# Kernel optimization log

Hardware: AMD Instinct MI355X
Metric: run time of the kernel (lower is better)

Reference implementation:

```python
import jax, jax.numpy as jnp
import numpy as np

N = 100000
E = 1600000
NIN = 128
NOUT = 128


def setup_inputs() -> dict:
    key = jax.random.key(0)
    k1, k2, k3, k4 = jax.random.split(key, 4)
    x = jax.random.normal(k1, (N, NIN), dtype=jnp.float32)
    edge_index = jax.random.randint(k2, (2, E), 0, N, dtype=jnp.int64)
    edge_attr = jnp.ones((E,), dtype=jnp.float32)  # unused by GCNConv
    # PyG Linear weight is [out, in]; glorot-ish init
    W = jax.random.normal(k3, (NOUT, NIN), dtype=jnp.float32) / np.sqrt(NIN)
    b = jnp.zeros((NOUT,), dtype=jnp.float32)
    return {"x": x, "edge_index": edge_index, "edge_attr": edge_attr, "W": W, "b": b}


def reference(x, edge_index, edge_attr, W, b):
    # PyG GCNConv: add self-loops, symmetric degree normalization,
    # linear transform, scatter-add aggregation at destination, + bias.
    n = x.shape[0]
    loops = jnp.arange(n, dtype=edge_index.dtype)
    src = jnp.concatenate([edge_index[0], loops])  # [E+N]
    dst = jnp.concatenate([edge_index[1], loops])  # [E+N]
    # degree over destination (col) including self-loops, edge weight = 1
    deg = jax.ops.segment_sum(jnp.ones_like(dst, dtype=x.dtype), dst, num_segments=n)
    dinv = jnp.where(deg > 0, jax.lax.rsqrt(deg), 0.0)
    norm = dinv[src] * dinv[dst]  # [E+N]
    h = x @ W.T  # [N, NOUT]
    msg = h[src] * norm[:, None]  # [E+N, NOUT]
    out = jax.ops.segment_sum(msg, dst, num_segments=n)  # [N, NOUT]
    return out + b
```

## Files before the change

kernel.cpp:

```cpp
#include <hip/hip_runtime.h>

#define TPB 256
#define NBLK 256
#define BSH 8

typedef __attribute__((ext_vector_type(4))) float f32x4;
typedef __attribute__((ext_vector_type(8))) short short8;

__device__ __forceinline__ unsigned short f2bf(float f) {
    unsigned u = __float_as_uint(f);
    u = (u + 0x7fffu + ((u >> 16) & 1u)) >> 16;
    return (unsigned short)u;
}
__device__ __forceinline__ float bflo(unsigned u) { return __uint_as_float(u << 16); }
__device__ __forceinline__ float bfhi(unsigned u) { return __uint_as_float(u & 0xffff0000u); }


__global__ __launch_bounds__(256) void k_bhist(const int* __restrict__ dst,
                                               int* __restrict__ btotal, int E, int NB) {
    __shared__ int sh[512];
    for (int i = threadIdx.x; i < NB; i += 256) sh[i] = 0;
    __syncthreads();
    int chunk = (E + NBLK - 1) / NBLK;
    int lo = blockIdx.x * chunk;
    int hi = min(E, lo + chunk);
    for (int e = lo + threadIdx.x; e < hi; e += 256)
        atomicAdd(&sh[dst[e] >> BSH], 1);
    __syncthreads();
    for (int i = threadIdx.x; i < NB; i += 256)
        if (sh[i]) atomicAdd(&btotal[i], sh[i]);
}


__global__ __launch_bounds__(512) void k_bscan(const int* __restrict__ btotal,
                                               int* __restrict__ bbase, int* __restrict__ bcur,
                                               int* __restrict__ offsets, int E, int NB, int N) {
    __shared__ int tmp[2][512];
    int t = threadIdx.x;
    int v = (t < NB) ? btotal[t] : 0;
    tmp[0][t] = v;
    __syncthreads();
    int sb = 0;
    for (int d = 1; d < 512; d <<= 1) {
        int val = tmp[sb][t];
        if (t >= d) val += tmp[sb][t - d];
        tmp[sb ^ 1][t] = val;
        sb ^= 1;
        __syncthreads();
    }
    int excl = tmp[sb][t] - v;
    if (t < NB) { bbase[t] = excl; bcur[t] = excl; }
    if (t == 0) { bbase[NB] = E; offsets[N] = E; }
}


__global__ __launch_bounds__(256) void k_bscatter(const int* __restrict__ src,
                                                  const int* __restrict__ dst,
                                                  int* __restrict__ bcur,
                                                  int2* __restrict__ pairs, int E, int NB) {
    __shared__ int sh[512];
    __shared__ int sbase[512];
    for (int i = threadIdx.x; i < NB; i += 256) sh[i] = 0;
    __syncthreads();
    int chunk = (E + NBLK - 1) / NBLK;
    int lo = blockIdx.x * chunk;
    int hi = min(E, lo + chunk);
    for (int e = lo + threadIdx.x; e < hi; e += 256)
        atomicAdd(&sh[dst[e] >> BSH], 1);
    __syncthreads();
    for (int i = threadIdx.x; i < NB; i += 256) {
        int c = sh[i];
        sbase[i] = c ? atomicAdd(&bcur[i], c) : 0;
    }
    __syncthreads();
    for (int i = threadIdx.x; i < NB; i += 256) sh[i] = sbase[i];
    __syncthreads();
    for (int e = lo + threadIdx.x; e < hi; e += 256) {
        int d = dst[e];
        int pos = atomicAdd(&sh[d >> BSH], 1);
        pairs[pos] = make_int2(d, src[e]);
    }
}


__global__ __launch_bounds__(256) void k_bcsr(const int2* __restrict__ pairs,
                                              const int* __restrict__ bbase,
                                              int* __restrict__ offsets,
                                              int* __restrict__ sorted_src,
                                              float* __restrict__ dinv, int N) {
    __shared__ int hist[256];
    __shared__ int tmp[2][256];
    __shared__ int scur[256];
    int b = blockIdx.x;
    int s0 = bbase[b], s1 = bbase[b + 1];
    int t = threadIdx.x;
    hist[t] = 0;
    __syncthreads();
    for (int e = s0 + t; e < s1; e += 256)
        atomicAdd(&hist[pairs[e].x & 255], 1);
    __syncthreads();
    int v = hist[t];
    tmp[0][t] = v;
    __syncthreads();
    int sb = 0;
    for (int d = 1; d < 256; d <<= 1) {
        int val = tmp[sb][t];
        if (t >= d) val += tmp[sb][t - d];
        tmp[sb ^ 1][t] = val;
        sb ^= 1;
        __syncthreads();
    }
    int gbase = s0 + (tmp[sb][t] - v);
    scur[t] = gbase;
    int d = (b << BSH) + t;
    if (d < N) { offsets[d] = gbase; dinv[d] = rsqrtf((float)v + 1.0f); }
    __syncthreads();
    for (int e = s0 + t; e < s1; e += 256) {
        int2 pr = pairs[e];
        int pos = atomicAdd(&scur[pr.x & 255], 1);
        sorted_src[pos] = pr.y;
    }
}


__global__ void k_castW(const float* __restrict__ W, unsigned short* __restrict__ Wt) {
    int i = blockIdx.x * TPB + threadIdx.x;
    if (i < 128 * 128) Wt[i] = f2bf(W[i]);
}


__global__ __launch_bounds__(256) void k_gemm(const float* __restrict__ x,
                                              const unsigned short* __restrict__ Wt,
                                              const float* __restrict__ dinv,
                                              unsigned short* __restrict__ g, int n) {
    __shared__ unsigned short wb[128][136];
    const int tid = threadIdx.x;

    for (int chunk = tid; chunk < 2048; chunk += 256) {
        int nrow = chunk >> 4, k8 = (chunk & 15) << 3;
        *(uint4*)&wb[nrow][k8] = ((const uint4*)Wt)[chunk];
    }
    __syncthreads();

    const int lane = tid & 63;
    const int wid  = tid >> 6;
    const int l15  = lane & 15;
    const int quad = lane >> 4;
    const int row  = blockIdx.x * 64 + wid * 16 + l15;
    const int rowc = (row < n) ? row : (n - 1);

    f32x4 acc[8];
    #pragma unroll
    for (int t = 0; t < 8; ++t) acc[t] = (f32x4){0.f, 0.f, 0.f, 0.f};

    #pragma unroll
    for (int ks = 0; ks < 4; ++ks) {
        const int kb = ks * 32 + quad * 8;
        float4 a0 = *(const float4*)(x + (long)rowc * 128 + kb);
        float4 a1 = *(const float4*)(x + (long)rowc * 128 + kb + 4);
        union { unsigned short u[8]; short8 v; } af;
        af.u[0] = f2bf(a0.x); af.u[1] = f2bf(a0.y); af.u[2] = f2bf(a0.z); af.u[3] = f2bf(a0.w);
        af.u[4] = f2bf(a1.x); af.u[5] = f2bf(a1.y); af.u[6] = f2bf(a1.z); af.u[7] = f2bf(a1.w);
        #pragma unroll
        for (int t = 0; t < 8; ++t) {
            short8 bf = *(const short8*)&wb[t * 16 + l15][kb];
            acc[t] = __builtin_amdgcn_mfma_f32_16x16x32_bf16(af.v, bf, acc[t], 0, 0, 0);
        }
    }

    int   orow[4];
    float dv[4];
    #pragma unroll
    for (int r = 0; r < 4; ++r) {
        orow[r] = blockIdx.x * 64 + wid * 16 + quad * 4 + r;
        dv[r]   = (orow[r] < n) ? dinv[orow[r]] : 0.f;
    }
    #pragma unroll
    for (int t = 0; t < 8; ++t) {
        int col = t * 16 + l15;
        #pragma unroll
        for (int r = 0; r < 4; ++r) {
            if (orow[r] < n)
                g[(long)orow[r] * 128 + col] = f2bf(acc[t][r] * dv[r]);
        }
    }
}


__global__ __launch_bounds__(256) void k_aggregate(const int* __restrict__ sorted_src,
                                                   const int* __restrict__ offsets,
                                                   const unsigned short* __restrict__ g,
                                                   const float* __restrict__ dinv,
                                                   const float* __restrict__ b,
                                                   float* __restrict__ out, int n) {
    int d = blockIdx.x * (TPB / 32) + (threadIdx.x >> 5);
    if (d >= n) return;
    int c = (threadIdx.x & 31) << 2;

    int s0 = offsets[d];
    int s1 = offsets[d + 1];

    float4 acc = make_float4(0.f, 0.f, 0.f, 0.f);
    auto addrow = [&](int r) {
        uint2 p = *(const uint2*)(g + (long)r * 128 + c);
        acc.x += bflo(p.x); acc.y += bfhi(p.x);
        acc.z += bflo(p.y); acc.w += bfhi(p.y);
    };

    addrow(d);
    int e = s0;
    for (; e + 8 <= s1; e += 8) {
        int a[8];
        #pragma unroll
        for (int j = 0; j < 8; ++j) a[j] = sorted_src[e + j];
        #pragma unroll
        for (int j = 0; j < 8; ++j) addrow(a[j]);
    }
    for (; e + 4 <= s1; e += 4) {
        int a[4];
        #pragma unroll
        for (int j = 0; j < 4; ++j) a[j] = sorted_src[e + j];
        #pragma unroll
        for (int j = 0; j < 4; ++j) addrow(a[j]);
    }
    for (; e < s1; ++e) addrow(sorted_src[e]);

    float s = dinv[d];
    float4 bb = *(const float4*)(b + c);
    float4 r = make_float4(acc.x * s + bb.x, acc.y * s + bb.y,
                           acc.z * s + bb.z, acc.w * s + bb.w);
    *(float4*)(out + (long)d * 128 + c) = r;
}


extern "C" void kernel_launch(void* const* d_in, const int* in_sizes, int n_in,
                              void* d_out, int out_size, void* d_ws, size_t ws_size,
                              hipStream_t stream) {
    const float* x  = (const float*)d_in[0];
    const int*   ei = (const int*)d_in[1];
    const float* W  = (const float*)d_in[3];
    const float* b  = (const float*)d_in[4];
    float* out = (float*)d_out;

    const int N = in_sizes[0] / 128;
    const int E = in_sizes[1] / 2;
    const int* src = ei;
    const int* dst = ei + E;
    const int NB = (N + 255) >> BSH;

    char* p = (char*)d_ws;
    auto carve = [&](size_t bytes) { char* q = p; p += (bytes + 255) & ~(size_t)255; return q; };
    int*            btotal     = (int*)           carve(512 * 4);
    int*            bbase      = (int*)           carve(513 * 4);
    int*            bcur       = (int*)           carve(512 * 4);
    int*            offsets    = (int*)           carve((size_t)(N + 1) * 4);
    float*          dinv       = (float*)         carve((size_t)N * 4);
    int2*           pairs      = (int2*)          carve((size_t)E * 8);
    int*            sorted_src = (int*)           carve((size_t)E * 4);
    unsigned short* Wt         = (unsigned short*)carve((size_t)128 * 128 * 2);
    unsigned short* g          = (unsigned short*)carve((size_t)N * 128 * 2);

    hipMemsetAsync(btotal, 0, 512 * 4, stream);

    k_bhist   <<<NBLK, TPB, 0, stream>>>(dst, btotal, E, NB);
    k_bscan   <<<1, 512, 0, stream>>>(btotal, bbase, bcur, offsets, E, NB, N);
    k_bscatter<<<NBLK, TPB, 0, stream>>>(src, dst, bcur, pairs, E, NB);
    k_bcsr    <<<NB, TPB, 0, stream>>>(pairs, bbase, offsets, sorted_src, dinv, N);

    k_castW<<<(128 * 128 + TPB - 1) / TPB, TPB, 0, stream>>>(W, Wt);
    k_gemm<<<(N + 63) / 64, TPB, 0, stream>>>(x, Wt, dinv, g, N);

    k_aggregate<<<(N + (TPB / 32) - 1) / (TPB / 32), TPB, 0, stream>>>(
        sorted_src, offsets, g, dinv, b, out, N);
}
```

Measured before the change: 254.6 us.

## Drop memset and castW launches; per-block histograms; unroll aggregate by 16

The bucket histogram now writes per-block rows to a workspace that the scan kernel reduces, which removes the global atomics and the memset launch. The separate weight-cast kernel is removed and each GEMM block converts W to bf16 while loading it into shared memory. The aggregation inner loop now prefetches 16 neighbour indices per iteration instead of 8. Together these cut two launches and some atomics, in exchange for redundant W conversion in every GEMM block and a serial 256-row reduction in the single-block scan.

After: 254.9 us. About the same (+0.1%).

```diff
diff --git a/kernel.cpp b/kernel.cpp
--- a/kernel.cpp
+++ b/kernel.cpp
@@ -17,40 +17,44 @@
 
 
 __global__ __launch_bounds__(256) void k_bhist(const int* __restrict__ dst,
-                                               int* __restrict__ btotal, int E, int NB) {
+                                               int* __restrict__ blockhist, int E) {
     __shared__ int sh[512];
-    for (int i = threadIdx.x; i < NB; i += 256) sh[i] = 0;
+    int t = threadIdx.x;
+    sh[t] = 0; sh[t + 256] = 0;
     __syncthreads();
     int chunk = (E + NBLK - 1) / NBLK;
     int lo = blockIdx.x * chunk;
     int hi = min(E, lo + chunk);
-    for (int e = lo + threadIdx.x; e < hi; e += 256)
+    for (int e = lo + t; e < hi; e += 256)
         atomicAdd(&sh[dst[e] >> BSH], 1);
     __syncthreads();
-    for (int i = threadIdx.x; i < NB; i += 256)
-        if (sh[i]) atomicAdd(&btotal[i], sh[i]);
-}
-
-
-__global__ __launch_bounds__(512) void k_bscan(const int* __restrict__ btotal,
+    int* row = blockhist + blockIdx.x * 512;
+    row[t] = sh[t];
+    row[t + 256] = sh[t + 256];
+}
+
+
+__global__ __launch_bounds__(512) void k_bscan(const int* __restrict__ blockhist,
                                                int* __restrict__ bbase, int* __restrict__ bcur,
-                                               int* __restrict__ offsets, int E, int NB, int N) {
+                                               int* __restrict__ offsets, int E, int N) {
     __shared__ int tmp[2][512];
     int t = threadIdx.x;
-    int v = (t < NB) ? btotal[t] : 0;
-    tmp[0][t] = v;
+    int total = 0;
+    #pragma unroll 8
+    for (int b = 0; b < NBLK; ++b) total += blockhist[b * 512 + t];
+    tmp[0][t] = total;
     __syncthreads();
     int sb = 0;
     for (int d = 1; d < 512; d <<= 1) {
-        int val = tmp[sb][t];
-        if (t >= d) val += tmp[sb][t - d];
+        int val = tmp[sb][t] + ((t >= d) ? tmp[sb][t - d] : 0);
         tmp[sb ^ 1][t] = val;
         sb ^= 1;
         __syncthreads();
     }
-    int excl = tmp[sb][t] - v;
-    if (t < NB) { bbase[t] = excl; bcur[t] = excl; }
-    if (t == 0) { bbase[NB] = E; offsets[N] = E; }
+    int excl = tmp[sb][t] - total;
+    bbase[t] = excl;
+    bcur[t] = excl;
+    if (t == 0) { bbase[512] = E; offsets[N] = E; }
 }
 
 
@@ -60,22 +64,23 @@
                                                   int2* __restrict__ pairs, int E, int NB) {
     __shared__ int sh[512];
     __shared__ int sbase[512];
-    for (int i = threadIdx.x; i < NB; i += 256) sh[i] = 0;
+    int t = threadIdx.x;
+    sh[t] = 0; sh[t + 256] = 0;
     __syncthreads();
     int chunk = (E + NBLK - 1) / NBLK;
     int lo = blockIdx.x * chunk;
     int hi = min(E, lo + chunk);
-    for (int e = lo + threadIdx.x; e < hi; e += 256)
+    for (int e = lo + t; e < hi; e += 256)
         atomicAdd(&sh[dst[e] >> BSH], 1);
     __syncthreads();
-    for (int i = threadIdx.x; i < NB; i += 256) {
+    for (int i = t; i < NB; i += 256) {
         int c = sh[i];
         sbase[i] = c ? atomicAdd(&bcur[i], c) : 0;
     }
     __syncthreads();
-    for (int i = threadIdx.x; i < NB; i += 256) sh[i] = sbase[i];
-    __syncthreads();
-    for (int e = lo + threadIdx.x; e < hi; e += 256) {
+    for (int i = t; i < NB; i += 256) sh[i] = sbase[i];
+    __syncthreads();
+    for (int e = lo + t; e < hi; e += 256) {
         int d = dst[e];
         int pos = atomicAdd(&sh[d >> BSH], 1);
         pairs[pos] = make_int2(d, src[e]);
@@ -104,8 +109,7 @@
     __syncthreads();
     int sb = 0;
     for (int d = 1; d < 256; d <<= 1) {
-        int val = tmp[sb][t];
-        if (t >= d) val += tmp[sb][t - d];
+        int val = tmp[sb][t] + ((t >= d) ? tmp[sb][t - d] : 0);
         tmp[sb ^ 1][t] = val;
         sb ^= 1;
         __syncthreads();
@@ -123,14 +127,8 @@
 }
 
 
-__global__ void k_castW(const float* __restrict__ W, unsigned short* __restrict__ Wt) {
-    int i = blockIdx.x * TPB + threadIdx.x;
-    if (i < 128 * 128) Wt[i] = f2bf(W[i]);
-}
-
-
 __global__ __launch_bounds__(256) void k_gemm(const float* __restrict__ x,
-                                              const unsigned short* __restrict__ Wt,
+                                              const float* __restrict__ W,
                                               const float* __restrict__ dinv,
                                               unsigned short* __restrict__ g, int n) {
     __shared__ unsigned short wb[128][136];
@@ -138,7 +136,13 @@
 
     for (int chunk = tid; chunk < 2048; chunk += 256) {
         int nrow = chunk >> 4, k8 = (chunk & 15) << 3;
-        *(uint4*)&wb[nrow][k8] = ((const uint4*)Wt)[chunk];
+        const float* wp = W + nrow * 128 + k8;
+        float4 w0 = *(const float4*)wp;
+        float4 w1 = *(const float4*)(wp + 4);
+        union { unsigned short u[8]; uint4 q; } pk;
+        pk.u[0] = f2bf(w0.x); pk.u[1] = f2bf(w0.y); pk.u[2] = f2bf(w0.z); pk.u[3] = f2bf(w0.w);
+        pk.u[4] = f2bf(w1.x); pk.u[5] = f2bf(w1.y); pk.u[6] = f2bf(w1.z); pk.u[7] = f2bf(w1.w);
+        *(uint4*)&wb[nrow][k8] = pk.q;
     }
     __syncthreads();
 
@@ -209,12 +213,12 @@
 
     addrow(d);
     int e = s0;
-    for (; e + 8 <= s1; e += 8) {
-        int a[8];
-        #pragma unroll
-        for (int j = 0; j < 8; ++j) a[j] = sorted_src[e + j];
-        #pragma unroll
-        for (int j = 0; j < 8; ++j) addrow(a[j]);
+    for (; e + 16 <= s1; e += 16) {
+        int a[16];
+        #pragma unroll
+        for (int j = 0; j < 16; ++j) a[j] = sorted_src[e + j];
+        #pragma unroll
+        for (int j = 0; j < 16; ++j) addrow(a[j]);
     }
     for (; e + 4 <= s1; e += 4) {
         int a[4];
@@ -250,25 +254,21 @@
 
     char* p = (char*)d_ws;
     auto carve = [&](size_t bytes) { char* q = p; p += (bytes + 255) & ~(size_t)255; return q; };
-    int*            btotal     = (int*)           carve(512 * 4);
+    int*            blockhist  = (int*)           carve((size_t)NBLK * 512 * 4);
     int*            bbase      = (int*)           carve(513 * 4);
     int*            bcur       = (int*)           carve(512 * 4);
     int*            offsets    = (int*)           carve((size_t)(N + 1) * 4);
     float*          dinv       = (float*)         carve((size_t)N * 4);
     int2*           pairs      = (int2*)          carve((size_t)E * 8);
     int*            sorted_src = (int*)           carve((size_t)E * 4);
-    unsigned short* Wt         = (unsigned short*)carve((size_t)128 * 128 * 2);
     unsigned short* g          = (unsigned short*)carve((size_t)N * 128 * 2);
 
-    hipMemsetAsync(btotal, 0, 512 * 4, stream);
-
-    k_bhist   <<<NBLK, TPB, 0, stream>>>(dst, btotal, E, NB);
-    k_bscan   <<<1, 512, 0, stream>>>(btotal, bbase, bcur, offsets, E, NB, N);
+    k_bhist   <<<NBLK, TPB, 0, stream>>>(dst, blockhist, E);
+    k_bscan   <<<1, 512, 0, stream>>>(blockhist, bbase, bcur, offsets, E, N);
     k_bscatter<<<NBLK, TPB, 0, stream>>>(src, dst, bcur, pairs, E, NB);
     k_bcsr    <<<NB, TPB, 0, stream>>>(pairs, bbase, offsets, sorted_src, dinv, N);
 
-    k_castW<<<(128 * 128 + TPB - 1) / TPB, TPB, 0, stream>>>(W, Wt);
-    k_gemm<<<(N + 63) / 64, TPB, 0, stream>>>(x, Wt, dinv, g, N);
+    k_gemm<<<(N + 63) / 64, TPB, 0, stream>>>(x, W, dinv, g, N);
 
     k_aggregate<<<(N + (TPB / 32) - 1) / (TPB / 32), TPB, 0, stream>>>(
         sorted_src, offsets, g, dinv, b, out, N);
```
